# Kernel tuning notes

Measured on AMD Instinct MI355X. Metric: run time of the kernel, lower is better.

The kernel has to match this reference:

```python
import jax, jax.numpy as jnp
import numpy as np

INIT_L = 512.0
EPS = 1e-6
N_HEAD = 16


def fire_bias(T, w1, b1, w2, b2, c, L_multiplier):
    # positions and relative distances
    pos = jnp.arange(T, dtype=jnp.float32)
    rel = pos[:, None] - pos[None, :]                      # (T, T)
    threshold = jnp.abs(L_multiplier * INIT_L)
    pos_norm = jnp.maximum(pos, threshold)[:, None]        # (T, 1)
    rel = jnp.log(jnp.abs(c * rel) + 1.0)                  # (T, T)
    pos_norm = jnp.log(jnp.abs(c * pos_norm) + 1.0) + EPS  # (T, 1)
    nd = rel / pos_norm                                    # (T, T)
    # tiny MLP: 1 -> mlp_width -> n_head
    h = jax.nn.relu(nd[..., None] * w1[0] + b1)            # (T, T, 32)
    bias = jnp.einsum('tsw,wh->hts', h, w2) + b2[:, None, None]  # (H, T, T)
    causal = jnp.tril(jnp.ones((T, T), dtype=bool))
    bias = jnp.where(causal[None], bias, -jnp.inf)
    return bias[None]                                      # (1, H, T, T)


def reference(x, Wqkv, bqkv, Wproj, bproj, w1, b1, w2, b2, c_param, L_multiplier):
    B, T, C = x.shape
    H = N_HEAD
    hd = C // H
    qkv = x @ Wqkv + bqkv                                  # (B, T, 3C)
    q, k, v = jnp.split(qkv, 3, axis=-1)
    q = q.reshape(B, T, H, hd).transpose(0, 2, 1, 3)       # (B, H, T, hd)
    k = k.reshape(B, T, H, hd).transpose(0, 2, 1, 3)
    v = v.reshape(B, T, H, hd).transpose(0, 2, 1, 3)
    bias = fire_bias(T, w1, b1, w2, b2, c_param, L_multiplier)  # (1, H, T, T)
    scale = 1.0 / jnp.sqrt(jnp.float32(hd))
    att = jnp.einsum('bhqd,bhkd->bhqk', q, k) * scale + bias
    att = jax.nn.softmax(att, axis=-1)
    y = jnp.einsum('bhqk,bhkd->bhqd', att, v)              # (B, H, T, hd)
    y = y.transpose(0, 2, 1, 3).reshape(B, T, C)
    return y @ Wproj + bproj


def setup_inputs() -> dict:
    key = jax.random.key(0)
    ks = jax.random.split(key, 8)
    B, T, C, H, W = 2, 2048, 1024, 16, 32
    s = 0.02
    return {
        'x': jax.random.normal(ks[0], (B, T, C), jnp.float32),
        'Wqkv': jax.random.normal(ks[1], (C, 3 * C), jnp.float32) * s,
        'bqkv': jnp.zeros((3 * C,), jnp.float32),
        'Wproj': jax.random.normal(ks[2], (C, C), jnp.float32) * s,
        'bproj': jnp.zeros((C,), jnp.float32),
        'w1': jax.random.normal(ks[3], (1, W), jnp.float32),
        'b1': jnp.zeros((W,), jnp.float32),
        'w2': jax.random.normal(ks[4], (W, H), jnp.float32) * 0.1,
        'b2': jnp.zeros((H,), jnp.float32),
        'c_param': jnp.float32(0.1),
        'L_multiplier': jnp.float32(1.0),
    }
```

## Files before the change

kernel.cpp:

```cpp
#include <hip/hip_runtime.h>
#include <cstdint>

typedef unsigned short u16;
typedef unsigned int u32;

typedef short bf16x8 __attribute__((ext_vector_type(8)));
typedef float f32x4 __attribute__((ext_vector_type(4)));

#define LN2 0.69314718055994530942f
#define LOG2E 1.44269504088896340736f
#define INFF __builtin_inff()

__device__ __forceinline__ u16 f2bf(float f) {
  u32 u = __float_as_uint(f);
  u = (u + 0x7fffu + ((u >> 16) & 1u)) >> 16;
  return (u16)u;
}
__device__ __forceinline__ u32 pack2bf(float a, float b) {
  u32 ta = __float_as_uint(a) + 0x8000u;
  u32 tb = __float_as_uint(b) + 0x8000u;
  return __builtin_amdgcn_perm(tb, ta, 0x07060302u);
}

#if __has_builtin(__builtin_amdgcn_global_load_lds)
#define HAVE_GLDS 1
__device__ __forceinline__ void glds16(const u16* g, u16* l) {
  __builtin_amdgcn_global_load_lds((const __attribute__((address_space(1))) void*)g,
                                   (__attribute__((address_space(3))) void*)l, 16, 0, 0);
}
#else
#define HAVE_GLDS 0
#endif


__global__ void k_convert_x(const float* __restrict__ in, u16* __restrict__ out, int n4) {
  int i = blockIdx.x * blockDim.x + threadIdx.x;
  if (i < n4) {
    float4 v = ((const float4*)in)[i];
    ushort4 o;
    o.x = f2bf(v.x); o.y = f2bf(v.y); o.z = f2bf(v.z); o.w = f2bf(v.w);
    ((ushort4*)out)[i] = o;
  }
}

__global__ void k_transpose_bf(const float* __restrict__ in, u16* __restrict__ out, int R, int C) {
  __shared__ float t[32][33];
  int c0 = blockIdx.x * 32, r0 = blockIdx.y * 32;
  int tx = threadIdx.x, ty = threadIdx.y;
#pragma unroll
  for (int k = 0; k < 4; k++) t[ty + 8 * k][tx] = in[(size_t)(r0 + ty + 8 * k) * C + c0 + tx];
  __syncthreads();
#pragma unroll
  for (int k = 0; k < 4; k++) out[(size_t)(c0 + ty + 8 * k) * R + r0 + tx] = f2bf(t[tx][ty + 8 * k]);
}

__global__ void k_tables(const float* __restrict__ cP, const float* __restrict__ lP,
                         float* __restrict__ ig2, float* __restrict__ rl) {
  int t = blockIdx.x * blockDim.x + threadIdx.x;
  float c = fabsf(cP[0]);
  if (t < 2048) {
    float lm = lP[0];
    float thr = fabsf(lm * 512.0f);
    float pn = fmaxf((float)t, thr);
    float den = logf(c * pn + 1.0f) + 1e-6f;
    ig2[t] = LN2 / den;
  }
  if (t < 2112) {
    int d = t - 63;
    if (d < 0) d = 0;
    rl[t] = log2f(c * (float)d + 1.0f);
  }
}

__global__ void k_segments(const float* __restrict__ w1, const float* __restrict__ b1,
                           const float* __restrict__ w2, const float* __restrict__ b2,
                           float* __restrict__ segX, float* __restrict__ segA,
                           float* __restrict__ segB, int* __restrict__ segU) {
  __shared__ float xs[32];
  __shared__ float srt[32];
  __shared__ float uniq[32];
  __shared__ int uCnt;
  int t = threadIdx.x;
  if (t < 32) {
    float w = w1[t], b = b1[t];
    xs[t] = (w != 0.0f) ? (-b / w) : INFF;
  }
  __syncthreads();
  if (t < 32) {
    float x = xs[t];
    int r = 0;
    for (int v = 0; v < 32; v++) {
      float xv = xs[v];
      if (xv < x || (xv == x && v < t)) r++;
    }
    srt[r] = x;
  }
  __syncthreads();
  if (t == 0) {
    int u = 0;
    for (int i = 0; i < 32; i++) {
      float v = srt[i];
      if (v < 3.0e38f && (u == 0 || v != uniq[u - 1])) uniq[u++] = v;
    }
    uCnt = u;
    segU[0] = u;
  }
  __syncthreads();
  int u = uCnt;
  if (t < u) segX[t] = uniq[t];
  for (int idx = t; idx < (u + 1) * 16; idx += blockDim.x) {
    int j = idx >> 4, h = idx & 15;
    float p;
    if (u == 0) p = 0.0f;
    else if (j == 0) p = uniq[0] - 1.0f;
    else if (j == u) p = uniq[u - 1] + 1.0f;
    else p = 0.5f * (uniq[j - 1] + uniq[j]);
    float A = b2[h], B = 0.0f;
    for (int w = 0; w < 32; w++) {
      float w1w = w1[w], b1w = b1[w], w2wh = w2[w * 16 + h];
      if (w1w != 0.0f) {
        if (fmaf(w1w, p, b1w) > 0.0f) { B += w1w * w2wh; A += b1w * w2wh; }
      } else if (b1w > 0.0f) {
        A += b1w * w2wh;
      }
    }
    segA[j * 16 + h] = A;
    segB[j * 16 + h] = B;
  }
}

template <int MODE, int BN>
__launch_bounds__(256, 3)
__global__ void k_gemm(const u16* __restrict__ A, const u16* __restrict__ BT,
                       const float* __restrict__ bias, float* __restrict__ outF,
                       u16* __restrict__ outQ, u16* __restrict__ outK, u16* __restrict__ outV,
                       int M, int N, int K) {
  constexpr int NT = BN / 32;
  constexpr int NCH = BN / 32;
  __shared__ u16 As[128 * 64];
  __shared__ u16 Bs[BN * 64];
  const int tid = threadIdx.x;
  const int lane = tid & 63, wave = tid >> 6;
  const int li = lane & 15, quad = lane >> 4;
  const int wrow = (wave >> 1) * 64, wcol = (wave & 1) * (BN / 2);
  const int rb = blockIdx.y * 128, cb = blockIdx.x * BN;

  f32x4 acc[4][NT];
#pragma unroll
  for (int i = 0; i < 4; i++)
#pragma unroll
    for (int j = 0; j < NT; j++) acc[i][j] = (f32x4){0.f, 0.f, 0.f, 0.f};

#if HAVE_GLDS
  const u16* gA = A + (size_t)(rb + (tid >> 3)) * K + (tid & 7) * 8;
  const u16* gB = BT + (size_t)(cb + (tid >> 3)) * K + (tid & 7) * 8;
  u16* lA = As + wave * 512;
  u16* lB = Bs + wave * 512;

  for (int k0 = 0; k0 < K; k0 += 64) {
    __syncthreads();
#pragma unroll
    for (int ch = 0; ch < 4; ch++) glds16(gA + (size_t)ch * 32 * K + k0, lA + ch * 2048);
#pragma unroll
    for (int ch = 0; ch < NCH; ch++) glds16(gB + (size_t)ch * 32 * K + k0, lB + ch * 2048);
    __syncthreads();
#pragma unroll
    for (int c = 0; c < 2; c++) {
      bf16x8 af[4], bfr[NT];
#pragma unroll
      for (int mt = 0; mt < 4; mt++)
        af[mt] = *(const bf16x8*)(&As[(wrow + mt * 16 + li) * 64 + c * 32 + quad * 8]);
#pragma unroll
      for (int nt = 0; nt < NT; nt++)
        bfr[nt] = *(const bf16x8*)(&Bs[(wcol + nt * 16 + li) * 64 + c * 32 + quad * 8]);
#pragma unroll
      for (int mt = 0; mt < 4; mt++)
#pragma unroll
        for (int nt = 0; nt < NT; nt++)
          acc[mt][nt] = __builtin_amdgcn_mfma_f32_16x16x32_bf16(af[mt], bfr[nt], acc[mt][nt], 0, 0, 0);
    }
  }
#else
  for (int k0 = 0; k0 < K; k0 += 64) {
    __syncthreads();
    for (int idx = tid * 8; idx < 128 * 64; idx += 256 * 8) {
      int rr = idx >> 6, cc = idx & 63;
      *(uint4*)(&As[idx]) = *(const uint4*)(A + (size_t)(rb + rr) * K + k0 + cc);
    }
    for (int idx = tid * 8; idx < BN * 64; idx += 256 * 8) {
      int rr = idx >> 6, cc = idx & 63;
      *(uint4*)(&Bs[idx]) = *(const uint4*)(BT + (size_t)(cb + rr) * K + k0 + cc);
    }
    __syncthreads();
#pragma unroll
    for (int c = 0; c < 2; c++) {
      bf16x8 af[4], bfr[NT];
#pragma unroll
      for (int mt = 0; mt < 4; mt++)
        af[mt] = *(const bf16x8*)(&As[(wrow + mt * 16 + li) * 64 + c * 32 + quad * 8]);
#pragma unroll
      for (int nt = 0; nt < NT; nt++)
        bfr[nt] = *(const bf16x8*)(&Bs[(wcol + nt * 16 + li) * 64 + c * 32 + quad * 8]);
#pragma unroll
      for (int mt = 0; mt < 4; mt++)
#pragma unroll
        for (int nt = 0; nt < NT; nt++)
          acc[mt][nt] = __builtin_amdgcn_mfma_f32_16x16x32_bf16(af[mt], bfr[nt], acc[mt][nt], 0, 0, 0);
    }
  }
#endif

#pragma unroll
  for (int mt = 0; mt < 4; mt++)
#pragma unroll
    for (int nt = 0; nt < NT; nt++)
#pragma unroll
      for (int r = 0; r < 4; r++) {
        int row = rb + wrow + mt * 16 + quad * 4 + r;
        int col = cb + wcol + nt * 16 + li;
        float v = acc[mt][nt][r] + bias[col];
        if (MODE == 0) {
          int b = row >> 11, tt = row & 2047;
          int sel = col >> 10, w = col & 1023, h = w >> 6, dd = w & 63;
          u16* dst = (sel == 0) ? outQ : ((sel == 1) ? outK : outV);
          dst[(size_t)((b * 16 + h) * 2048 + tt) * 64 + dd] = f2bf(v);
        } else {
          outF[(size_t)row * N + col] = v;
        }
      }
}

__launch_bounds__(256, 3)
__global__ void k_attn(const u16* __restrict__ Q, const u16* __restrict__ K,
                       const u16* __restrict__ V, u16* __restrict__ Y,
                       const float* __restrict__ ig2, const float* __restrict__ RL,
                       const float* __restrict__ segX, const float* __restrict__ segA,
                       const float* __restrict__ segB, const int* __restrict__ segU) {
  __shared__ u16 Ks[64][72];
  __shared__ u16 Vts[64][72];
  __shared__ u16 Ps[64][72];
  __shared__ float rls[2112];
  __shared__ float sXl[32];
  __shared__ float sAl[33];
  __shared__ float sBl[33];

  const int pr = blockIdx.x, h = blockIdx.y, b = blockIdx.z;
  const int tid = threadIdx.x, lane = tid & 63, wave = tid >> 6;
  const int li = lane & 15, quad = lane >> 4;
  const int bh = b * 16 + h;
  const u16* Qg = Q + (size_t)bh * 2048 * 64;
  const u16* Kg = K + (size_t)bh * 2048 * 64;
  const u16* Vg = V + (size_t)bh * 2048 * 64;

  for (int i = tid; i < 2112; i += 256) rls[i] = RL[i];

  const int u = segU[0];
  float x0 = INFF, A0, B0, A1, B1;
  A0 = segA[h]; B0 = segB[h]; A1 = A0; B1 = B0;
  if (u == 1) { x0 = segX[0]; A1 = segA[16 + h]; B1 = segB[16 + h]; }
  if (u > 1) {
    if (tid < u) sXl[tid] = segX[tid];
    if (tid < u + 1) { sAl[tid] = segA[tid * 16 + h]; sBl[tid] = segB[tid * 16 + h]; }
  }
  const float A0e = A0 * LOG2E, A1e = A1 * LOG2E;
  const float SCL = 0.125f * LOG2E;

  auto run_tile = [&](int qt) {
    const int qw = qt * 64 + wave * 16;
    const int t = qw + li;
    bf16x8 qf[2];
#pragma unroll
    for (int c = 0; c < 2; c++)
      qf[c] = *(const bf16x8*)(Qg + (size_t)t * 64 + c * 32 + quad * 8);

    const float gI = ig2[t];
    const float x0r = x0 / gI;
    const float B0g = B0 * gI * LOG2E, B1g = B1 * gI * LOG2E;
    float mrow = -INFF, lrow = 0.0f;
    f32x4 oacc[4];
#pragma unroll
    for (int nt = 0; nt < 4; nt++) oacc[nt] = (f32x4){0.f, 0.f, 0.f, 0.f};

    uint4 kv0, kv1, w0, w1;
    {
      const u16* ksrc = Kg + (size_t)(tid >> 2) * 64 + (tid & 3) * 16;
      kv0 = *(const uint4*)(ksrc);
      kv1 = *(const uint4*)(ksrc + 8);
      const u16* vsrc = Vg + (size_t)(2 * (tid & 31)) * 64 + (tid >> 5) * 8;
      w0 = *(const uint4*)(vsrc);
      w1 = *(const uint4*)(vsrc + 64);
    }

    for (int kt = 0; kt <= qt; kt++) {
      const int kb = kt * 64;
      __syncthreads();
      *(uint4*)(&Ks[tid >> 2][(tid & 3) * 16]) = kv0;
      *(uint4*)(&Ks[tid >> 2][(tid & 3) * 16 + 8]) = kv1;
      {
        const int kkp = tid & 31, d0 = (tid >> 5) * 8;
        const u16* pw0 = (const u16*)&w0;
        const u16* pw1 = (const u16*)&w1;
#pragma unroll
        for (int j = 0; j < 8; j++)
          *(u32*)(&Vts[d0 + j][2 * kkp]) = (u32)pw0[j] | ((u32)pw1[j] << 16);
      }
      __syncthreads();
      if (kt < qt) {
        const u16* ksrc = Kg + (size_t)(kb + 64 + (tid >> 2)) * 64 + (tid & 3) * 16;
        kv0 = *(const uint4*)(ksrc);
        kv1 = *(const uint4*)(ksrc + 8);
        const u16* vsrc = Vg + (size_t)(kb + 64 + 2 * (tid & 31)) * 64 + (tid >> 5) * 8;
        w0 = *(const uint4*)(vsrc);
        w1 = *(const uint4*)(vsrc + 64);
      }

      f32x4 sacc[4];
#pragma unroll
      for (int nt = 0; nt < 4; nt++) sacc[nt] = (f32x4){0.f, 0.f, 0.f, 0.f};
#pragma unroll
      for (int c = 0; c < 2; c++)
#pragma unroll
        for (int nt = 0; nt < 4; nt++) {
          bf16x8 kf = *(const bf16x8*)(&Ks[nt * 16 + li][c * 32 + quad * 8]);
          sacc[nt] = __builtin_amdgcn_mfma_f32_16x16x32_bf16(kf, qf[c], sacc[nt], 0, 0, 0);
        }

      const int Cbase = t - kb - quad * 4 + 63;
      const float* rp = &rls[Cbase - 51];
      if (u <= 1) {
        const int lim = Cbase - 63;
#pragma unroll
        for (int nt = 0; nt < 4; nt++)
#pragma unroll
          for (int r = 0; r < 4; r++) {
            float rlv = rp[51 - nt * 16 - r];
            bool hi = rlv > x0r;
            float z = fmaf(rlv, hi ? B1g : B0g, hi ? A1e : A0e);
            z = fmaf(sacc[nt][r], SCL, z);
            if (kt == qt) z = (nt * 16 + r > lim) ? -INFF : z;
            sacc[nt][r] = z;
          }
      } else {
        const int lim = Cbase - 63;
#pragma unroll
        for (int nt = 0; nt < 4; nt++)
#pragma unroll
          for (int r = 0; r < 4; r++) {
            float nd = rp[51 - nt * 16 - r] * gI;
            int j = 0;
            for (int i = 0; i < u; i++) j += (nd > sXl[i]) ? 1 : 0;
            float z = (fmaf(nd, sBl[j], sAl[j]) + sacc[nt][r] * 0.125f) * LOG2E;
            if (kt == qt) z = (nt * 16 + r > lim) ? -INFF : z;
            sacc[nt][r] = z;
          }
      }

      float vm = -INFF;
#pragma unroll
      for (int nt = 0; nt < 4; nt++)
#pragma unroll
        for (int r = 0; r < 4; r++) vm = fmaxf(vm, sacc[nt][r]);
      vm = fmaxf(vm, __shfl_xor(vm, 16, 64));
      vm = fmaxf(vm, __shfl_xor(vm, 32, 64));
      float mnew = fmaxf(mrow, vm);
      float alpha = __builtin_amdgcn_exp2f(mrow - mnew);
      mrow = mnew;
      float s = 0.0f;
#pragma unroll
      for (int nt = 0; nt < 4; nt++)
#pragma unroll
        for (int r = 0; r < 4; r++) {
          float p = __builtin_amdgcn_exp2f(sacc[nt][r] - mnew);
          sacc[nt][r] = p;
          s += p;
        }
      s += __shfl_xor(s, 16, 64);
      s += __shfl_xor(s, 32, 64);
      lrow = lrow * alpha + s;
#pragma unroll
      for (int nt = 0; nt < 4; nt++)
#pragma unroll
        for (int r = 0; r < 4; r++) oacc[nt][r] *= alpha;

      const int prow = wave * 16 + li;
#pragma unroll
      for (int nt = 0; nt < 4; nt++) {
        uint2 pk;
        pk.x = pack2bf(sacc[nt][0], sacc[nt][1]);
        pk.y = pack2bf(sacc[nt][2], sacc[nt][3]);
        *(uint2*)(&Ps[prow][nt * 16 + quad * 4]) = pk;
      }

#pragma unroll
      for (int c = 0; c < 2; c++) {
        bf16x8 pf = *(const bf16x8*)(&Ps[wave * 16 + li][c * 32 + quad * 8]);
#pragma unroll
        for (int nt = 0; nt < 4; nt++) {
          bf16x8 vf = *(const bf16x8*)(&Vts[nt * 16 + li][c * 32 + quad * 8]);
          oacc[nt] = __builtin_amdgcn_mfma_f32_16x16x32_bf16(vf, pf, oacc[nt], 0, 0, 0);
        }
      }
    }

    float inv = 1.0f / lrow;
    u16* dst = Y + (size_t)(b * 2048 + t) * 1024 + h * 64 + quad * 4;
#pragma unroll
    for (int nt = 0; nt < 4; nt++) {
      uint2 pk;
      pk.x = pack2bf(oacc[nt][0] * inv, oacc[nt][1] * inv);
      pk.y = pack2bf(oacc[nt][2] * inv, oacc[nt][3] * inv);
      *(uint2*)(dst + nt * 16) = pk;
    }
  };

  run_tile(pr);
  run_tile(31 - pr);
}

extern "C" void kernel_launch(void* const* d_in, const int* in_sizes, int n_in,
                              void* d_out, int out_size, void* d_ws, size_t ws_size,
                              hipStream_t stream) {
  (void)in_sizes; (void)n_in; (void)out_size; (void)ws_size;
  const float* x = (const float*)d_in[0];
  const float* Wqkv = (const float*)d_in[1];
  const float* bqkv = (const float*)d_in[2];
  const float* Wproj = (const float*)d_in[3];
  const float* bproj = (const float*)d_in[4];
  const float* w1 = (const float*)d_in[5];
  const float* b1 = (const float*)d_in[6];
  const float* w2 = (const float*)d_in[7];
  const float* b2 = (const float*)d_in[8];
  const float* cP = (const float*)d_in[9];
  const float* lP = (const float*)d_in[10];

  char* ws = (char*)d_ws;
  u16* Xbf = (u16*)(ws);
  u16* WqkvT = (u16*)(ws + (size_t)(8 << 20));
  u16* WprojT = (u16*)(ws + (size_t)(14 << 20));
  u16* Qb = (u16*)(ws + (size_t)(16 << 20));
  u16* Kb = (u16*)(ws + (size_t)(24 << 20));
  u16* Vb = (u16*)(ws + (size_t)(32 << 20));
  u16* Yb = (u16*)(ws + (size_t)(40 << 20));
  float* IG = (float*)(ws + (size_t)(48 << 20));
  float* RL = IG + 2048;
  float* SEGX = RL + 2112;
  float* SEGA = SEGX + 32;
  float* SEGB = SEGA + 33 * 16;
  int* SEGU = (int*)(SEGB + 33 * 16);

  k_convert_x<<<4096, 256, 0, stream>>>(x, Xbf, 1048576);
  k_transpose_bf<<<dim3(96, 32), dim3(32, 8), 0, stream>>>(Wqkv, WqkvT, 1024, 3072);
  k_transpose_bf<<<dim3(32, 32), dim3(32, 8), 0, stream>>>(Wproj, WprojT, 1024, 1024);
  k_tables<<<9, 256, 0, stream>>>(cP, lP, IG, RL);
  k_segments<<<1, 64, 0, stream>>>(w1, b1, w2, b2, SEGX, SEGA, SEGB, SEGU);

  k_gemm<0, 128><<<dim3(24, 32), 256, 0, stream>>>(Xbf, WqkvT, bqkv, nullptr, Qb, Kb, Vb,
                                                   4096, 3072, 1024);
  k_attn<<<dim3(16, 16, 2), 256, 0, stream>>>(Qb, Kb, Vb, Yb, IG, RL, SEGX, SEGA, SEGB, SEGU);
  k_gemm<1, 64><<<dim3(16, 32), 256, 0, stream>>>(Yb, WprojT, bproj, (float*)d_out, nullptr,
                                                  nullptr, nullptr, 4096, 1024, 1024);
}
```

Measured before the change: 233.0 us.

## Split attention work one q-tile per block, swizzle LDS, skip redundant rescale

Each attention block now processes a single 64-row query tile instead of a balanced pair, doubling the grid to 1024 blocks. The tile order is interleaved by head parity so long and short causal tiles mix across the schedule. LDS arrays drop their padding in favour of an XOR swizzle to avoid bank conflicts. The output rescale is skipped when no row max grew, and the max and sum reductions become tree-shaped. Occupancy hint rises to 4 blocks per CU. This trades the static pairing balance for more blocks and relies on the hardware scheduler to even out the causal imbalance.

```diff
diff --git a/kernel.cpp b/kernel.cpp
--- a/kernel.cpp
+++ b/kernel.cpp
@@ -31,6 +31,10 @@
 #else
 #define HAVE_GLDS 0
 #endif
+
+__device__ __forceinline__ u16* swzp(u16* base, int row, int bc) {
+  return (u16*)((char*)base + row * 128 + (bc ^ ((row & 7) << 4)));
+}
 
 
 __global__ void k_convert_x(const float* __restrict__ in, u16* __restrict__ out, int n4) {
@@ -230,21 +234,25 @@
       }
 }
 
-__launch_bounds__(256, 3)
+__launch_bounds__(256, 4)
 __global__ void k_attn(const u16* __restrict__ Q, const u16* __restrict__ K,
                        const u16* __restrict__ V, u16* __restrict__ Y,
                        const float* __restrict__ ig2, const float* __restrict__ RL,
                        const float* __restrict__ segX, const float* __restrict__ segA,
                        const float* __restrict__ segB, const int* __restrict__ segU) {
-  __shared__ u16 Ks[64][72];
-  __shared__ u16 Vts[64][72];
-  __shared__ u16 Ps[64][72];
+  __shared__ u16 Ks[64 * 64];
+  __shared__ u16 Vts[64 * 64];
+  __shared__ u16 Ps[64 * 64];
   __shared__ float rls[2112];
   __shared__ float sXl[32];
   __shared__ float sAl[33];
   __shared__ float sBl[33];
 
-  const int pr = blockIdx.x, h = blockIdx.y, b = blockIdx.z;
+  const int xi = blockIdx.x, h = blockIdx.y, b = blockIdx.z;
+  const int q0b = xi >> 1;
+  const int flip = (xi & 1) ^ ((h >> 3) & 1);
+  const int qt = flip ? (31 - q0b) : q0b;
+
   const int tid = threadIdx.x, lane = tid & 63, wave = tid >> 6;
   const int li = lane & 15, quad = lane >> 4;
   const int bh = b * 16 + h;
@@ -265,156 +273,155 @@
   const float A0e = A0 * LOG2E, A1e = A1 * LOG2E;
   const float SCL = 0.125f * LOG2E;
 
-  auto run_tile = [&](int qt) {
-    const int qw = qt * 64 + wave * 16;
-    const int t = qw + li;
-    bf16x8 qf[2];
-#pragma unroll
-    for (int c = 0; c < 2; c++)
-      qf[c] = *(const bf16x8*)(Qg + (size_t)t * 64 + c * 32 + quad * 8);
-
-    const float gI = ig2[t];
-    const float x0r = x0 / gI;
-    const float B0g = B0 * gI * LOG2E, B1g = B1 * gI * LOG2E;
-    float mrow = -INFF, lrow = 0.0f;
-    f32x4 oacc[4];
-#pragma unroll
-    for (int nt = 0; nt < 4; nt++) oacc[nt] = (f32x4){0.f, 0.f, 0.f, 0.f};
-
-    uint4 kv0, kv1, w0, w1;
+  const int qw = qt * 64 + wave * 16;
+  const int t = qw + li;
+  bf16x8 qf[2];
+#pragma unroll
+  for (int c = 0; c < 2; c++)
+    qf[c] = *(const bf16x8*)(Qg + (size_t)t * 64 + c * 32 + quad * 8);
+
+  const float gI = ig2[t];
+  const float x0r = x0 / gI;
+  const float B0g = B0 * gI * LOG2E, B1g = B1 * gI * LOG2E;
+  float mrow = -INFF, lrow = 0.0f;
+  f32x4 oacc[4];
+#pragma unroll
+  for (int nt = 0; nt < 4; nt++) oacc[nt] = (f32x4){0.f, 0.f, 0.f, 0.f};
+
+  uint4 kv0, kv1, w0, w1;
+  {
+    const u16* ksrc = Kg + (size_t)(tid >> 2) * 64 + (tid & 3) * 16;
+    kv0 = *(const uint4*)(ksrc);
+    kv1 = *(const uint4*)(ksrc + 8);
+    const u16* vsrc = Vg + (size_t)(2 * (tid & 31)) * 64 + (tid >> 5) * 8;
+    w0 = *(const uint4*)(vsrc);
+    w1 = *(const uint4*)(vsrc + 64);
+  }
+
+  const int krow = tid >> 2, kcol = (tid & 3) * 32;
+  const int kkp = tid & 31, d0v = (tid >> 5) * 8;
+
+  for (int kt = 0; kt <= qt; kt++) {
+    const int kb = kt * 64;
+    __syncthreads();
+    *(uint4*)swzp(Ks, krow, kcol) = kv0;
+    *(uint4*)swzp(Ks, krow, kcol + 16) = kv1;
     {
-      const u16* ksrc = Kg + (size_t)(tid >> 2) * 64 + (tid & 3) * 16;
+      const u16* pw0 = (const u16*)&w0;
+      const u16* pw1 = (const u16*)&w1;
+#pragma unroll
+      for (int j = 0; j < 8; j++)
+        *(u32*)swzp(Vts, d0v + j, 4 * kkp) = (u32)pw0[j] | ((u32)pw1[j] << 16);
+    }
+    __syncthreads();
+    if (kt < qt) {
+      const u16* ksrc = Kg + (size_t)(kb + 64 + (tid >> 2)) * 64 + (tid & 3) * 16;
       kv0 = *(const uint4*)(ksrc);
       kv1 = *(const uint4*)(ksrc + 8);
-      const u16* vsrc = Vg + (size_t)(2 * (tid & 31)) * 64 + (tid >> 5) * 8;
+      const u16* vsrc = Vg + (size_t)(kb + 64 + 2 * (tid & 31)) * 64 + (tid >> 5) * 8;
       w0 = *(const uint4*)(vsrc);
       w1 = *(const uint4*)(vsrc + 64);
     }
 
-    for (int kt = 0; kt <= qt; kt++) {
-      const int kb = kt * 64;
-      __syncthreads();
-      *(uint4*)(&Ks[tid >> 2][(tid & 3) * 16]) = kv0;
-      *(uint4*)(&Ks[tid >> 2][(tid & 3) * 16 + 8]) = kv1;
-      {
-        const int kkp = tid & 31, d0 = (tid >> 5) * 8;
-        const u16* pw0 = (const u16*)&w0;
-        const u16* pw1 = (const u16*)&w1;
-#pragma unroll
-        for (int j = 0; j < 8; j++)
-          *(u32*)(&Vts[d0 + j][2 * kkp]) = (u32)pw0[j] | ((u32)pw1[j] << 16);
+    f32x4 sacc[4];
+#pragma unroll
+    for (int nt = 0; nt < 4; nt++) sacc[nt] = (f32x4){0.f, 0.f, 0.f, 0.f};
+#pragma unroll
+    for (int c = 0; c < 2; c++)
+#pragma unroll
+      for (int nt = 0; nt < 4; nt++) {
+        bf16x8 kf = *(const bf16x8*)swzp(Ks, nt * 16 + li, c * 64 + quad * 16);
+        sacc[nt] = __builtin_amdgcn_mfma_f32_16x16x32_bf16(kf, qf[c], sacc[nt], 0, 0, 0);
       }
-      __syncthreads();
-      if (kt < qt) {
-        const u16* ksrc = Kg + (size_t)(kb + 64 + (tid >> 2)) * 64 + (tid & 3) * 16;
-        kv0 = *(const uint4*)(ksrc);
-        kv1 = *(const uint4*)(ksrc + 8);
-        const u16* vsrc = Vg + (size_t)(kb + 64 + 2 * (tid & 31)) * 64 + (tid >> 5) * 8;
-        w0 = *(const uint4*)(vsrc);
-        w1 = *(const uint4*)(vsrc + 64);
-      }
-
-      f32x4 sacc[4];
-#pragma unroll
-      for (int nt = 0; nt < 4; nt++) sacc[nt] = (f32x4){0.f, 0.f, 0.f, 0.f};
-#pragma unroll
-      for (int c = 0; c < 2; c++)
-#pragma unroll
-        for (int nt = 0; nt < 4; nt++) {
-          bf16x8 kf = *(const bf16x8*)(&Ks[nt * 16 + li][c * 32 + quad * 8]);
-          sacc[nt] = __builtin_amdgcn_mfma_f32_16x16x32_bf16(kf, qf[c], sacc[nt], 0, 0, 0);
+
+    const int Cbase = t - kb - quad * 4 + 63;
+    const float* rp = &rls[Cbase - 51];
+    if (u <= 1) {
+      const int lim = Cbase - 63;
+#pragma unroll
+      for (int nt = 0; nt < 4; nt++)
+#pragma unroll
+        for (int r = 0; r < 4; r++) {
+          float rlv = rp[51 - nt * 16 - r];
+          bool hi = rlv > x0r;
+          float z = fmaf(rlv, hi ? B1g : B0g, hi ? A1e : A0e);
+          z = fmaf(sacc[nt][r], SCL, z);
+          if (kt == qt) z = (nt * 16 + r > lim) ? -INFF : z;
+          sacc[nt][r] = z;
         }
-
-      const int Cbase = t - kb - quad * 4 + 63;
-      const float* rp = &rls[Cbase - 51];
-      if (u <= 1) {
-        const int lim = Cbase - 63;
-#pragma unroll
-        for (int nt = 0; nt < 4; nt++)
-#pragma unroll
-          for (int r = 0; r < 4; r++) {
-            float rlv = rp[51 - nt * 16 - r];
-            bool hi = rlv > x0r;
-            float z = fmaf(rlv, hi ? B1g : B0g, hi ? A1e : A0e);
-            z = fmaf(sacc[nt][r], SCL, z);
-            if (kt == qt) z = (nt * 16 + r > lim) ? -INFF : z;
-            sacc[nt][r] = z;
-          }
-      } else {
-        const int lim = Cbase - 63;
-#pragma unroll
-        for (int nt = 0; nt < 4; nt++)
-#pragma unroll
-          for (int r = 0; r < 4; r++) {
-            float nd = rp[51 - nt * 16 - r] * gI;
-            int j = 0;
-            for (int i = 0; i < u; i++) j += (nd > sXl[i]) ? 1 : 0;
-            float z = (fmaf(nd, sBl[j], sAl[j]) + sacc[nt][r] * 0.125f) * LOG2E;
-            if (kt == qt) z = (nt * 16 + r > lim) ? -INFF : z;
-            sacc[nt][r] = z;
-          }
-      }
-
-      float vm = -INFF;
+    } else {
+      const int lim = Cbase - 63;
 #pragma unroll
       for (int nt = 0; nt < 4; nt++)
 #pragma unroll
-        for (int r = 0; r < 4; r++) vm = fmaxf(vm, sacc[nt][r]);
-      vm = fmaxf(vm, __shfl_xor(vm, 16, 64));
-      vm = fmaxf(vm, __shfl_xor(vm, 32, 64));
-      float mnew = fmaxf(mrow, vm);
-      float alpha = __builtin_amdgcn_exp2f(mrow - mnew);
-      mrow = mnew;
-      float s = 0.0f;
+        for (int r = 0; r < 4; r++) {
+          float nd = rp[51 - nt * 16 - r] * gI;
+          int j = 0;
+          for (int i = 0; i < u; i++) j += (nd > sXl[i]) ? 1 : 0;
+          float z = (fmaf(nd, sBl[j], sAl[j]) + sacc[nt][r] * 0.125f) * LOG2E;
+          if (kt == qt) z = (nt * 16 + r > lim) ? -INFF : z;
+          sacc[nt][r] = z;
+        }
+    }
+
+    f32x4 mm = sacc[0];
+#pragma unroll
+    for (int nt = 1; nt < 4; nt++)
+#pragma unroll
+      for (int r = 0; r < 4; r++) mm[r] = fmaxf(mm[r], sacc[nt][r]);
+    float vm = fmaxf(fmaxf(mm[0], mm[1]), fmaxf(mm[2], mm[3]));
+    vm = fmaxf(vm, __shfl_xor(vm, 16, 64));
+    vm = fmaxf(vm, __shfl_xor(vm, 32, 64));
+    float mnew = fmaxf(mrow, vm);
+    bool grew = mnew > mrow;
+    float alpha = __builtin_amdgcn_exp2f(mrow - mnew);
+    mrow = mnew;
+#pragma unroll
+    for (int nt = 0; nt < 4; nt++)
+#pragma unroll
+      for (int r = 0; r < 4; r++)
+        sacc[nt][r] = __builtin_amdgcn_exp2f(sacc[nt][r] - mnew);
+    f32x4 sv = (sacc[0] + sacc[1]) + (sacc[2] + sacc[3]);
+    float s = (sv[0] + sv[1]) + (sv[2] + sv[3]);
+    s += __shfl_xor(s, 16, 64);
+    s += __shfl_xor(s, 32, 64);
+    lrow = lrow * alpha + s;
+    if (__any(grew)) {
 #pragma unroll
       for (int nt = 0; nt < 4; nt++)
 #pragma unroll
-        for (int r = 0; r < 4; r++) {
-          float p = __builtin_amdgcn_exp2f(sacc[nt][r] - mnew);
-          sacc[nt][r] = p;
-          s += p;
-        }
-      s += __shfl_xor(s, 16, 64);
-      s += __shfl_xor(s, 32, 64);
-      lrow = lrow * alpha + s;
-#pragma unroll
-      for (int nt = 0; nt < 4; nt++)
-#pragma unroll
         for (int r = 0; r < 4; r++) oacc[nt][r] *= alpha;
-
-      const int prow = wave * 16 + li;
-#pragma unroll
-      for (int nt = 0; nt < 4; nt++) {
-        uint2 pk;
-        pk.x = pack2bf(sacc[nt][0], sacc[nt][1]);
-        pk.y = pack2bf(sacc[nt][2], sacc[nt][3]);
-        *(uint2*)(&Ps[prow][nt * 16 + quad * 4]) = pk;
-      }
-
-#pragma unroll
-      for (int c = 0; c < 2; c++) {
-        bf16x8 pf = *(const bf16x8*)(&Ps[wave * 16 + li][c * 32 + quad * 8]);
-#pragma unroll
-        for (int nt = 0; nt < 4; nt++) {
-          bf16x8 vf = *(const bf16x8*)(&Vts[nt * 16 + li][c * 32 + quad * 8]);
-          oacc[nt] = __builtin_amdgcn_mfma_f32_16x16x32_bf16(vf, pf, oacc[nt], 0, 0, 0);
-        }
-      }
-    }
-
-    float inv = 1.0f / lrow;
-    u16* dst = Y + (size_t)(b * 2048 + t) * 1024 + h * 64 + quad * 4;
+    }
+
+    const int prow = wave * 16 + li;
 #pragma unroll
     for (int nt = 0; nt < 4; nt++) {
       uint2 pk;
-      pk.x = pack2bf(oacc[nt][0] * inv, oacc[nt][1] * inv);
-      pk.y = pack2bf(oacc[nt][2] * inv, oacc[nt][3] * inv);
-      *(uint2*)(dst + nt * 16) = pk;
-    }
-  };
-
-  run_tile(pr);
-  run_tile(31 - pr);
+      pk.x = pack2bf(sacc[nt][0], sacc[nt][1]);
+      pk.y = pack2bf(sacc[nt][2], sacc[nt][3]);
+      *(uint2*)swzp(Ps, prow, 32 * nt + 8 * quad) = pk;
+    }
+
+#pragma unroll
+    for (int c = 0; c < 2; c++) {
+      bf16x8 pf = *(const bf16x8*)swzp(Ps, prow, c * 64 + quad * 16);
+#pragma unroll
+      for (int nt = 0; nt < 4; nt++) {
+        bf16x8 vf = *(const bf16x8*)swzp(Vts, nt * 16 + li, c * 64 + quad * 16);
+        oacc[nt] = __builtin_amdgcn_mfma_f32_16x16x32_bf16(vf, pf, oacc[nt], 0, 0, 0);
+      }
+    }
+  }
+
+  float inv = 1.0f / lrow;
+  u16* dst = Y + (size_t)(b * 2048 + t) * 1024 + h * 64 + quad * 4;
+#pragma unroll
+  for (int nt = 0; nt < 4; nt++) {
+    uint2 pk;
+    pk.x = pack2bf(oacc[nt][0] * inv, oacc[nt][1] * inv);
+    pk.y = pack2bf(oacc[nt][2] * inv, oacc[nt][3] * inv);
+    *(uint2*)(dst + nt * 16) = pk;
+  }
 }
 
 extern "C" void kernel_launch(void* const* d_in, const int* in_sizes, int n_in,
@@ -456,7 +463,7 @@
 
   k_gemm<0, 128><<<dim3(24, 32), 256, 0, stream>>>(Xbf, WqkvT, bqkv, nullptr, Qb, Kb, Vb,
                                                    4096, 3072, 1024);
-  k_attn<<<dim3(16, 16, 2), 256, 0, stream>>>(Qb, Kb, Vb, Yb, IG, RL, SEGX, SEGA, SEGB, SEGU);
+  k_attn<<<dim3(32, 16, 2), 256, 0, stream>>>(Qb, Kb, Vb, Yb, IG, RL, SEGX, SEGA, SEGB, SEGU);
   k_gemm<1, 64><<<dim3(16, 32), 256, 0, stream>>>(Yb, WprojT, bproj, (float*)d_out, nullptr,
                                                   nullptr, nullptr, 4096, 1024, 1024);
 }
```

Result: slower. 272.6 us (+17.0%).
